# Kernel tuning notes

Measured on AMD Instinct MI355X. Metric: run time of the kernel, lower is better.

## Reference

```python
import jax, jax.numpy as jnp
import numpy as np

B, N, C, HEADS, SR = 4, 16384, 64, 2, 8
SIDE = 128            # sqrt(N)
NKV = (SIDE // SR) ** 2  # 256
D = C // HEADS
LN_EPS = 1e-5


def setup_inputs() -> dict:
    key = jax.random.key(0)
    ks = jax.random.split(key, 12)
    s = 0.02
    return {
        "x": jax.random.normal(ks[0], (B, N, C), jnp.float32),
        "pos_2D": jax.random.uniform(ks[1], (B, HEADS, N, NKV), jnp.float32),
        "q_w": jax.random.normal(ks[2], (C, C), jnp.float32) * s,
        "q_b": jnp.zeros((C,), jnp.float32),
        "kv_w": jax.random.normal(ks[3], (2 * C, C), jnp.float32) * s,
        "kv_b": jnp.zeros((2 * C,), jnp.float32),
        "proj_w": jax.random.normal(ks[4], (C, C), jnp.float32) * s,
        "proj_b": jnp.zeros((C,), jnp.float32),
        "sr_w": jax.random.normal(ks[5], (C, C, SR, SR), jnp.float32) * s,  # OIHW
        "sr_b": jnp.zeros((C,), jnp.float32),
        "ln_g": jnp.ones((C,), jnp.float32),
        "ln_b": jnp.zeros((C,), jnp.float32),
        "alpha": jnp.full((1,), 0.3, jnp.float32),
    }


def reference(x, pos_2D, q_w, q_b, kv_w, kv_b, proj_w, proj_b, sr_w, sr_b, ln_g, ln_b, alpha):
    scale = D ** -0.5
    # q projection -> [B, HEADS, N, D]
    q = (jnp.einsum("bnc,oc->bno", x, q_w) + q_b).reshape(B, N, HEADS, D).transpose(0, 2, 1, 3)
    # spatial reduction: conv stride SR on [B, C, SIDE, SIDE]
    xs = x.transpose(0, 2, 1).reshape(B, C, SIDE, SIDE)
    xs = jax.lax.conv_general_dilated(
        xs, sr_w, window_strides=(SR, SR), padding="VALID",
        dimension_numbers=("NCHW", "OIHW", "NCHW")) + sr_b[None, :, None, None]
    xs = xs.reshape(B, C, NKV).transpose(0, 2, 1)  # [B, NKV, C]
    # LayerNorm over channels
    mu = jnp.mean(xs, axis=-1, keepdims=True)
    var = jnp.mean(jnp.square(xs - mu), axis=-1, keepdims=True)
    xs = (xs - mu) * jax.lax.rsqrt(var + LN_EPS) * ln_g + ln_b
    # kv projection -> k, v each [B, HEADS, NKV, D]
    kv = (jnp.einsum("bmc,oc->bmo", xs, kv_w) + kv_b).reshape(B, NKV, 2, HEADS, D)
    kv = kv.transpose(2, 0, 3, 1, 4)
    k, v = kv[0], kv[1]
    # attention with post-softmax positional blend
    attn = jax.nn.softmax(jnp.einsum("bhnd,bhmd->bhnm", q, k) * scale, axis=-1)
    a = alpha[0]
    attn = (1.0 - a) * attn + a * pos_2D
    out = jnp.einsum("bhnm,bhmd->bhnd", attn, v)
    out = out.transpose(0, 2, 1, 3).reshape(B, N, C)
    return jnp.einsum("bnc,oc->bno", out, proj_w) + proj_b
```

## Files before the change

### kernel.cpp

```cpp
#include <hip/hip_runtime.h>
#include <cstdint>
#include <cstddef>

#define NN 16384
#define CC 64
#define LN_EPS 1e-5f

typedef __attribute__((ext_vector_type(8))) short short8;
typedef __attribute__((ext_vector_type(4))) float f32x4;
typedef unsigned short ushort_t;
typedef unsigned int uint32;

__device__ __forceinline__ ushort_t f2bf(float f) {
  union { float f; uint32 u; } v; v.f = f;
  return (ushort_t)((v.u + 0x8000u) >> 16);
}
__device__ __forceinline__ uint32 pk2(float a, float b) {
  union { float f; uint32 u; } x, y; x.f = a; y.f = b;
  return ((x.u + 0x8000u) >> 16) | ((y.u + 0x8000u) & 0xffff0000u);
}
__device__ __forceinline__ short8 pk8(float4 a, float4 b) {
  union { short8 s; uint32 u[4]; } r;
  r.u[0] = pk2(a.x, a.y); r.u[1] = pk2(a.z, a.w);
  r.u[2] = pk2(b.x, b.y); r.u[3] = pk2(b.z, b.w);
  return r.s;
}

__global__ void prep_kernel(const float* __restrict__ sr_w, float* __restrict__ w2T,
                            float* __restrict__ conv_acc) {
  int tid = blockIdx.x * 256 + threadIdx.x;
  if (tid < 64*64*64) {
    int j = tid >> 6, o = tid & 63;
    int i = j & 63, kw = (j >> 6) & 7, kh = j >> 9;
    w2T[tid] = sr_w[o*4096 + i*64 + kh*8 + kw];
  } else {
    int e = tid - 64*64*64;
    if (e < 1024*64) conv_acc[e] = 0.0f;
  }
}

__global__ __launch_bounds__(256) void conv_kernel(const float* __restrict__ x,
                                                   const float* __restrict__ w2T,
                                                   float* __restrict__ conv_acc) {
  __shared__ float A_lds[32*132];
  __shared__ float W_lds[128*64];
  int t = threadIdx.x;
  int pt = blockIdx.x >> 5, kc = blockIdx.x & 31;
  int kh = kc >> 2, kw0 = (kc & 3) * 2;
  const float4* wsrc = (const float4*)(w2T + kc*128*64);
  float4* wdst = (float4*)W_lds;
  #pragma unroll
  for (int v = 0; v < 8; ++v) wdst[t + v*256] = wsrc[t + v*256];
  #pragma unroll
  for (int v = 0; v < 4; ++v) {
    int idx = v*1024 + t*4;
    int pl = idx >> 7, off = idx & 127;
    int p = pt*32 + pl;
    int b = p >> 8, rem = p & 255, ph = rem >> 4, pw = rem & 15;
    int n0 = (ph*8 + kh)*128 + pw*8 + kw0;
    *(float4*)&A_lds[pl*132 + off] = *(const float4*)&x[(b*NN + n0)*CC + off];
  }
  __syncthreads();
  int og = t & 15, pp = t >> 4;
  float acc[8] = {0,0,0,0,0,0,0,0};
  #pragma unroll 8
  for (int k = 0; k < 128; ++k) {
    float4 w4 = *(const float4*)&W_lds[k*64 + og*4];
    float a0 = A_lds[pp*264 + k];
    float a1 = A_lds[pp*264 + 132 + k];
    acc[0] += a0*w4.x; acc[1] += a0*w4.y; acc[2] += a0*w4.z; acc[3] += a0*w4.w;
    acc[4] += a1*w4.x; acc[5] += a1*w4.y; acc[6] += a1*w4.z; acc[7] += a1*w4.w;
  }
  int p0 = pt*32 + pp*2;
  #pragma unroll
  for (int j2 = 0; j2 < 4; ++j2) {
    atomicAdd(&conv_acc[p0*64 + og*4 + j2], acc[j2]);
    atomicAdd(&conv_acc[(p0+1)*64 + og*4 + j2], acc[4+j2]);
  }
}

__global__ __launch_bounds__(256) void lnkv_kernel(const float* __restrict__ conv_acc,
    const float* __restrict__ sr_b, const float* __restrict__ ln_g, const float* __restrict__ ln_b,
    const float* __restrict__ kv_w, const float* __restrict__ kv_b,
    ushort_t* __restrict__ k_out, ushort_t* __restrict__ v_out) {
  __shared__ float xsrow[4][64];
  int t = threadIdx.x;
  int w = t >> 6, lane = t & 63;
  float4 wk[16], wv[16];
  #pragma unroll
  for (int c4 = 0; c4 < 16; ++c4) {
    wk[c4] = *(const float4*)&kv_w[lane*64 + c4*4];
    wv[c4] = *(const float4*)&kv_w[(64+lane)*64 + c4*4];
  }
  float kb0 = kv_b[lane], kb1 = kv_b[64+lane];
  float sb = sr_b[lane], lg = ln_g[lane], lb = ln_b[lane];
  int h = lane >> 5, dd = lane & 31;
  for (int i = 0; i < 8; ++i) {
    int row = blockIdx.x*32 + w*8 + i;
    float xc = conv_acc[row*64 + lane] + sb;
    float s = xc;
    #pragma unroll
    for (int m = 1; m < 64; m <<= 1) s += __shfl_xor(s, m);
    float mu = s * (1.0f/64.0f);
    float d0 = xc - mu;
    float vs = d0*d0;
    #pragma unroll
    for (int m = 1; m < 64; m <<= 1) vs += __shfl_xor(vs, m);
    float rs = rsqrtf(vs*(1.0f/64.0f) + LN_EPS);
    xsrow[w][lane] = d0*rs*lg + lb;
    __syncthreads();
    float acc0 = kb0, acc1 = kb1;
    #pragma unroll
    for (int c4 = 0; c4 < 16; ++c4) {
      float4 xv = *(const float4*)&xsrow[w][c4*4];
      acc0 += xv.x*wk[c4].x + xv.y*wk[c4].y + xv.z*wk[c4].z + xv.w*wk[c4].w;
      acc1 += xv.x*wv[c4].x + xv.y*wv[c4].y + xv.z*wv[c4].z + xv.w*wv[c4].w;
    }
    int b = row >> 8, m2 = row & 255;
    int bh = b*2 + h;
    k_out[(bh*256 + m2)*32 + dd] = f2bf(acc0);
    v_out[(bh*32 + dd)*256 + m2] = f2bf(acc1);
    __syncthreads();
  }
}

__global__ __launch_bounds__(256) void qproj_kernel(const float* __restrict__ x,
    const float* __restrict__ q_w, const float* __restrict__ q_b, ushort_t* __restrict__ q_out) {
  int t = threadIdx.x;
  int w = t >> 6, lane = t & 63;
  int quad = lane >> 4, col = lane & 15;
  const float qscale = 0.17677669529663687f * 1.4426950408889634f;
  short8 bf[4][2];
  float qb[4];
  #pragma unroll
  for (int ct = 0; ct < 4; ++ct) {
    #pragma unroll
    for (int ksb = 0; ksb < 2; ++ksb) {
      const float* src = &q_w[(ct*16 + col)*64 + ksb*32 + quad*8];
      bf[ct][ksb] = pk8(*(const float4*)src, *(const float4*)(src + 4));
    }
    qb[ct] = q_b[ct*16 + col];
  }
  int rows0 = blockIdx.x*64 + w*16;
  int arow = rows0 + col;
  const float* xs = &x[(size_t)arow*64];
  short8 af0 = pk8(*(const float4*)&xs[quad*8],      *(const float4*)&xs[quad*8 + 4]);
  short8 af1 = pk8(*(const float4*)&xs[32 + quad*8], *(const float4*)&xs[36 + quad*8]);
  const f32x4 zero = {0.f, 0.f, 0.f, 0.f};
  #pragma unroll
  for (int ct = 0; ct < 4; ++ct) {
    f32x4 acc = __builtin_amdgcn_mfma_f32_16x16x32_bf16(af0, bf[ct][0], zero, 0, 0, 0);
    acc = __builtin_amdgcn_mfma_f32_16x16x32_bf16(af1, bf[ct][1], acc, 0, 0, 0);
    int o = ct*16 + col;
    int bh_hi = o >> 5, dd = o & 31;
    #pragma unroll
    for (int r = 0; r < 4; ++r) {
      int gr = rows0 + quad*4 + r;
      int b = gr >> 14, n = gr & 16383;
      q_out[((size_t)(b*2 + bh_hi)*NN + n)*32 + dd] = f2bf((acc[r] + qb[ct]) * qscale);
    }
  }
}

__global__ __launch_bounds__(256, 2) void attn_kernel(const ushort_t* __restrict__ q_ws,
    const ushort_t* __restrict__ k_ws, const ushort_t* __restrict__ v_ws,
    const float* __restrict__ pos, const float* __restrict__ alpha,
    ushort_t* __restrict__ attnout) {
  __shared__ __align__(16) ushort_t k_lds[256*40];
  __shared__ __align__(16) ushort_t v_lds[32*264];
  __shared__ __align__(16) ushort_t p_lds[4][16*256];
  int t = threadIdx.x;
  int bh = blockIdx.x >> 6, blk = blockIdx.x & 63;
  int b = bh >> 1, h = bh & 1;
  {
    const uint4* ksrc = (const uint4*)(k_ws + bh*8192);
    const uint4* vsrc = (const uint4*)(v_ws + bh*8192);
    uint4* kd = (uint4*)k_lds; uint4* vd = (uint4*)v_lds;
    #pragma unroll
    for (int vv = 0; vv < 4; ++vv) {
      int i = t + vv*256;
      kd[(i >> 2)*5 + (i & 3)] = ksrc[i];
      vd[(i >> 5)*33 + (i & 31)] = vsrc[i];
    }
  }
  __syncthreads();
  int w = t >> 6, lane = t & 63, quad = lane >> 4, col = lane & 15;
  float a = alpha[0];
  float one_minus_a = 1.0f - a;
  const f32x4 zero = {0.f, 0.f, 0.f, 0.f};
  for (int it = 0; it < 4; ++it) {
    int n0 = blk*256 + (it*4 + w)*16;
    short8 qa = *(const short8*)&q_ws[((size_t)bh*NN + n0 + col)*32 + quad*8];
    f32x4 st[16];
    #pragma unroll
    for (int tt = 0; tt < 16; ++tt) {
      short8 kb = *(const short8*)&k_lds[(tt*16 + col)*40 + quad*8];
      st[tt] = __builtin_amdgcn_mfma_f32_16x16x32_bf16(qa, kb, zero, 0, 0, 0);
    }
    #pragma unroll
    for (int r = 0; r < 4; ++r) {
      float mx = st[0][r];
      #pragma unroll
      for (int tt = 1; tt < 16; ++tt) mx = fmaxf(mx, st[tt][r]);
      #pragma unroll
      for (int m = 1; m < 16; m <<= 1) mx = fmaxf(mx, __shfl_xor(mx, m));
      float sum = 0.f;
      #pragma unroll
      for (int tt = 0; tt < 16; ++tt) {
        float e = __builtin_amdgcn_exp2f(st[tt][r] - mx);
        st[tt][r] = e; sum += e;
      }
      #pragma unroll
      for (int m = 1; m < 16; m <<= 1) sum += __shfl_xor(sum, m);
      float coef = one_minus_a * __builtin_amdgcn_rcpf(sum);
      int row = quad*4 + r;
      #pragma unroll
      for (int tt = 0; tt < 16; ++tt) {
        float av = st[tt][r]*coef;
        int colg = tt*16 + col;
        int u = colg >> 3, within = colg & 7;
        int usw = u ^ (row & 7);
        p_lds[w][row*256 + usw*8 + within] = f2bf(av);
      }
    }
    float4 p4[16];
    const float* pbase = &pos[((size_t)bh*NN + n0 + col)*256 + quad*8];
    #pragma unroll
    for (int ks = 0; ks < 8; ++ks) {
      p4[ks*2]   = *(const float4*)(pbase + ks*32);
      p4[ks*2+1] = *(const float4*)(pbase + ks*32 + 4);
    }
    __syncthreads();
    f32x4 o0 = zero, o1 = zero, e0 = zero, e1 = zero;
    #pragma unroll
    for (int ks = 0; ks < 8; ++ks) {
      short8 pa  = *(const short8*)&p_lds[w][col*256 + (((ks*4 + quad) ^ (col & 7))*8)];
      short8 vb0 = *(const short8*)&v_lds[(col)*264 + ks*32 + quad*8];
      short8 vb1 = *(const short8*)&v_lds[(16 + col)*264 + ks*32 + quad*8];
      short8 pf  = pk8(p4[ks*2], p4[ks*2+1]);
      o0 = __builtin_amdgcn_mfma_f32_16x16x32_bf16(pa, vb0, o0, 0, 0, 0);
      o1 = __builtin_amdgcn_mfma_f32_16x16x32_bf16(pa, vb1, o1, 0, 0, 0);
      e0 = __builtin_amdgcn_mfma_f32_16x16x32_bf16(pf, vb0, e0, 0, 0, 0);
      e1 = __builtin_amdgcn_mfma_f32_16x16x32_bf16(pf, vb1, e1, 0, 0, 0);
    }
    #pragma unroll
    for (int r = 0; r < 4; ++r) {
      int q_row = n0 + quad*4 + r;
      int base = (b*NN + q_row)*64 + h*32;
      attnout[base + col]      = f2bf(o0[r] + a*e0[r]);
      attnout[base + 16 + col] = f2bf(o1[r] + a*e1[r]);
    }
  }
}

__global__ __launch_bounds__(256) void proj_kernel(const ushort_t* __restrict__ attnout,
    const float* __restrict__ proj_w, const float* __restrict__ proj_b, float* __restrict__ out) {
  int t = threadIdx.x;
  int w = t >> 6, lane = t & 63;
  int quad = lane >> 4, col = lane & 15;
  short8 bf[4][2];
  float pb[4];
  #pragma unroll
  for (int ct = 0; ct < 4; ++ct) {
    #pragma unroll
    for (int ksb = 0; ksb < 2; ++ksb) {
      const float* src = &proj_w[(ct*16 + col)*64 + ksb*32 + quad*8];
      bf[ct][ksb] = pk8(*(const float4*)src, *(const float4*)(src + 4));
    }
    pb[ct] = proj_b[ct*16 + col];
  }
  int rows0 = blockIdx.x*64 + w*16;
  int arow = rows0 + col;
  short8 af0 = *(const short8*)&attnout[(size_t)arow*64 + quad*8];
  short8 af1 = *(const short8*)&attnout[(size_t)arow*64 + 32 + quad*8];
  const f32x4 zero = {0.f, 0.f, 0.f, 0.f};
  #pragma unroll
  for (int ct = 0; ct < 4; ++ct) {
    f32x4 acc = __builtin_amdgcn_mfma_f32_16x16x32_bf16(af0, bf[ct][0], zero, 0, 0, 0);
    acc = __builtin_amdgcn_mfma_f32_16x16x32_bf16(af1, bf[ct][1], acc, 0, 0, 0);
    int o = ct*16 + col;
    #pragma unroll
    for (int r = 0; r < 4; ++r) {
      int gr = rows0 + quad*4 + r;
      out[(size_t)gr*64 + o] = acc[r] + pb[ct];
    }
  }
}

extern "C" void kernel_launch(void* const* d_in, const int* in_sizes, int n_in,
                              void* d_out, int out_size, void* d_ws, size_t ws_size,
                              hipStream_t stream) {
  const float* x      = (const float*)d_in[0];
  const float* pos    = (const float*)d_in[1];
  const float* q_w    = (const float*)d_in[2];
  const float* q_b    = (const float*)d_in[3];
  const float* kv_w   = (const float*)d_in[4];
  const float* kv_b   = (const float*)d_in[5];
  const float* proj_w = (const float*)d_in[6];
  const float* proj_b = (const float*)d_in[7];
  const float* sr_w   = (const float*)d_in[8];
  const float* sr_b   = (const float*)d_in[9];
  const float* ln_g   = (const float*)d_in[10];
  const float* ln_b   = (const float*)d_in[11];
  const float* alpha  = (const float*)d_in[12];
  float* out = (float*)d_out;

  char* ws = (char*)d_ws;
  float* conv_acc   = (float*)(ws);
  float* w2T        = (float*)(ws + (256u<<10));
  ushort_t* k_ws    = (ushort_t*)(ws + (1280u<<10));
  ushort_t* v_ws    = (ushort_t*)(ws + (1408u<<10));
  ushort_t* q_ws    = (ushort_t*)(ws + (1536u<<10));
  ushort_t* a_ws    = (ushort_t*)(ws + (9728u<<10));

  hipLaunchKernelGGL(prep_kernel,  dim3(1280), dim3(256), 0, stream, sr_w, w2T, conv_acc);
  hipLaunchKernelGGL(conv_kernel,  dim3(1024), dim3(256), 0, stream, x, w2T, conv_acc);
  hipLaunchKernelGGL(lnkv_kernel,  dim3(32),   dim3(256), 0, stream, conv_acc, sr_b, ln_g, ln_b, kv_w, kv_b, k_ws, v_ws);
  hipLaunchKernelGGL(qproj_kernel, dim3(1024), dim3(256), 0, stream, x, q_w, q_b, q_ws);
  hipLaunchKernelGGL(attn_kernel,  dim3(512),  dim3(256), 0, stream, q_ws, k_ws, v_ws, pos, alpha, a_ws);
  hipLaunchKernelGGL(proj_kernel,  dim3(1024), dim3(256), 0, stream, a_ws, proj_w, proj_b, out);
}
```

Before: 301.8 us.

## Replace conv atomics with partial buffers and coalesce q/attn/proj stores via LDS

The conv kernel now writes per-kernel-chunk partial sums to a 32-way partial buffer, and the LN/KV kernel reduces them, instead of using float atomics on a zeroed accumulator. q-projection, attention output and projection outputs are staged through LDS tiles so global stores become 16-byte coalesced writes. The attention output layout changes to per-head [bh,N,32], which proj reads. The pos_2D loads are hoisted ahead of the QK/softmax phase to overlap their latency, and a block barrier is removed. The trade-off is more workspace traffic (8MB of partials), a serial 32-way read in lnkv, and extra LDS usage in attention.

```diff
diff --git a/kernel.cpp b/kernel.cpp
--- a/kernel.cpp
+++ b/kernel.cpp
@@ -26,22 +26,16 @@
   return r.s;
 }
 
-__global__ void prep_kernel(const float* __restrict__ sr_w, float* __restrict__ w2T,
-                            float* __restrict__ conv_acc) {
+__global__ void prep_kernel(const float* __restrict__ sr_w, float* __restrict__ w2T) {
   int tid = blockIdx.x * 256 + threadIdx.x;
-  if (tid < 64*64*64) {
-    int j = tid >> 6, o = tid & 63;
-    int i = j & 63, kw = (j >> 6) & 7, kh = j >> 9;
-    w2T[tid] = sr_w[o*4096 + i*64 + kh*8 + kw];
-  } else {
-    int e = tid - 64*64*64;
-    if (e < 1024*64) conv_acc[e] = 0.0f;
-  }
+  int j = tid >> 6, o = tid & 63;
+  int i = j & 63, kw = (j >> 6) & 7, kh = j >> 9;
+  w2T[tid] = sr_w[o*4096 + i*64 + kh*8 + kw];
 }
 
 __global__ __launch_bounds__(256) void conv_kernel(const float* __restrict__ x,
                                                    const float* __restrict__ w2T,
-                                                   float* __restrict__ conv_acc) {
+                                                   float* __restrict__ part) {
   __shared__ float A_lds[32*132];
   __shared__ float W_lds[128*64];
   int t = threadIdx.x;
@@ -72,14 +66,14 @@
     acc[4] += a1*w4.x; acc[5] += a1*w4.y; acc[6] += a1*w4.z; acc[7] += a1*w4.w;
   }
   int p0 = pt*32 + pp*2;
-  #pragma unroll
-  for (int j2 = 0; j2 < 4; ++j2) {
-    atomicAdd(&conv_acc[p0*64 + og*4 + j2], acc[j2]);
-    atomicAdd(&conv_acc[(p0+1)*64 + og*4 + j2], acc[4+j2]);
-  }
-}
-
-__global__ __launch_bounds__(256) void lnkv_kernel(const float* __restrict__ conv_acc,
+  float* dst = &part[(size_t)kc*65536 + p0*64 + og*4];
+  float4 s0 = {acc[0], acc[1], acc[2], acc[3]};
+  float4 s1 = {acc[4], acc[5], acc[6], acc[7]};
+  *(float4*)dst = s0;
+  *(float4*)(dst + 64) = s1;
+}
+
+__global__ __launch_bounds__(256) void lnkv_kernel(const float* __restrict__ part,
     const float* __restrict__ sr_b, const float* __restrict__ ln_g, const float* __restrict__ ln_b,
     const float* __restrict__ kv_w, const float* __restrict__ kv_b,
     ushort_t* __restrict__ k_out, ushort_t* __restrict__ v_out) {
@@ -95,9 +89,11 @@
   float kb0 = kv_b[lane], kb1 = kv_b[64+lane];
   float sb = sr_b[lane], lg = ln_g[lane], lb = ln_b[lane];
   int h = lane >> 5, dd = lane & 31;
-  for (int i = 0; i < 8; ++i) {
-    int row = blockIdx.x*32 + w*8 + i;
-    float xc = conv_acc[row*64 + lane] + sb;
+  for (int i = 0; i < 2; ++i) {
+    int row = blockIdx.x*8 + w*2 + i;
+    float xc = sb;
+    #pragma unroll
+    for (int kc = 0; kc < 32; ++kc) xc += part[kc*65536 + row*64 + lane];
     float s = xc;
     #pragma unroll
     for (int m = 1; m < 64; m <<= 1) s += __shfl_xor(s, m);
@@ -108,7 +104,6 @@
     for (int m = 1; m < 64; m <<= 1) vs += __shfl_xor(vs, m);
     float rs = rsqrtf(vs*(1.0f/64.0f) + LN_EPS);
     xsrow[w][lane] = d0*rs*lg + lb;
-    __syncthreads();
     float acc0 = kb0, acc1 = kb1;
     #pragma unroll
     for (int c4 = 0; c4 < 16; ++c4) {
@@ -120,45 +115,51 @@
     int bh = b*2 + h;
     k_out[(bh*256 + m2)*32 + dd] = f2bf(acc0);
     v_out[(bh*32 + dd)*256 + m2] = f2bf(acc1);
-    __syncthreads();
   }
 }
 
 __global__ __launch_bounds__(256) void qproj_kernel(const float* __restrict__ x,
     const float* __restrict__ q_w, const float* __restrict__ q_b, ushort_t* __restrict__ q_out) {
+  __shared__ __align__(16) ushort_t q_tile[64*64];
   int t = threadIdx.x;
   int w = t >> 6, lane = t & 63;
   int quad = lane >> 4, col = lane & 15;
   const float qscale = 0.17677669529663687f * 1.4426950408889634f;
-  short8 bf[4][2];
+  short8 bfr[4][2];
   float qb[4];
   #pragma unroll
   for (int ct = 0; ct < 4; ++ct) {
     #pragma unroll
     for (int ksb = 0; ksb < 2; ++ksb) {
       const float* src = &q_w[(ct*16 + col)*64 + ksb*32 + quad*8];
-      bf[ct][ksb] = pk8(*(const float4*)src, *(const float4*)(src + 4));
+      bfr[ct][ksb] = pk8(*(const float4*)src, *(const float4*)(src + 4));
     }
     qb[ct] = q_b[ct*16 + col];
   }
-  int rows0 = blockIdx.x*64 + w*16;
-  int arow = rows0 + col;
+  int rows0 = blockIdx.x*64;
+  int arow = rows0 + w*16 + col;
   const float* xs = &x[(size_t)arow*64];
   short8 af0 = pk8(*(const float4*)&xs[quad*8],      *(const float4*)&xs[quad*8 + 4]);
   short8 af1 = pk8(*(const float4*)&xs[32 + quad*8], *(const float4*)&xs[36 + quad*8]);
   const f32x4 zero = {0.f, 0.f, 0.f, 0.f};
   #pragma unroll
   for (int ct = 0; ct < 4; ++ct) {
-    f32x4 acc = __builtin_amdgcn_mfma_f32_16x16x32_bf16(af0, bf[ct][0], zero, 0, 0, 0);
-    acc = __builtin_amdgcn_mfma_f32_16x16x32_bf16(af1, bf[ct][1], acc, 0, 0, 0);
-    int o = ct*16 + col;
-    int bh_hi = o >> 5, dd = o & 31;
-    #pragma unroll
-    for (int r = 0; r < 4; ++r) {
-      int gr = rows0 + quad*4 + r;
-      int b = gr >> 14, n = gr & 16383;
-      q_out[((size_t)(b*2 + bh_hi)*NN + n)*32 + dd] = f2bf((acc[r] + qb[ct]) * qscale);
-    }
+    f32x4 acc = __builtin_amdgcn_mfma_f32_16x16x32_bf16(af0, bfr[ct][0], zero, 0, 0, 0);
+    acc = __builtin_amdgcn_mfma_f32_16x16x32_bf16(af1, bfr[ct][1], acc, 0, 0, 0);
+    #pragma unroll
+    for (int r = 0; r < 4; ++r)
+      q_tile[(w*16 + quad*4 + r)*64 + ct*16 + col] = f2bf((acc[r] + qb[ct]) * qscale);
+  }
+  __syncthreads();
+  int u = t;
+  #pragma unroll
+  for (int s = 0; s < 2; ++s, u += 256) {
+    int row = u >> 3, seg = u & 7;
+    int h2 = seg >> 2, sg = seg & 3;
+    uint4 val = *(const uint4*)&q_tile[row*64 + seg*8];
+    int gr = rows0 + row;
+    int b2 = gr >> 14, n = gr & 16383;
+    *(uint4*)&q_out[((size_t)(b2*2 + h2)*NN + n)*32 + sg*8] = val;
   }
 }
 
@@ -169,9 +170,9 @@
   __shared__ __align__(16) ushort_t k_lds[256*40];
   __shared__ __align__(16) ushort_t v_lds[32*264];
   __shared__ __align__(16) ushort_t p_lds[4][16*256];
+  __shared__ __align__(16) ushort_t o_lds[4][16*32];
   int t = threadIdx.x;
   int bh = blockIdx.x >> 6, blk = blockIdx.x & 63;
-  int b = bh >> 1, h = bh & 1;
   {
     const uint4* ksrc = (const uint4*)(k_ws + bh*8192);
     const uint4* vsrc = (const uint4*)(v_ws + bh*8192);
@@ -190,6 +191,13 @@
   const f32x4 zero = {0.f, 0.f, 0.f, 0.f};
   for (int it = 0; it < 4; ++it) {
     int n0 = blk*256 + (it*4 + w)*16;
+    float4 p4[16];
+    const float* pbase = &pos[((size_t)bh*NN + n0 + col)*256 + quad*8];
+    #pragma unroll
+    for (int ks = 0; ks < 8; ++ks) {
+      p4[ks*2]   = *(const float4*)(pbase + ks*32);
+      p4[ks*2+1] = *(const float4*)(pbase + ks*32 + 4);
+    }
     short8 qa = *(const short8*)&q_ws[((size_t)bh*NN + n0 + col)*32 + quad*8];
     f32x4 st[16];
     #pragma unroll
@@ -223,14 +231,6 @@
         p_lds[w][row*256 + usw*8 + within] = f2bf(av);
       }
     }
-    float4 p4[16];
-    const float* pbase = &pos[((size_t)bh*NN + n0 + col)*256 + quad*8];
-    #pragma unroll
-    for (int ks = 0; ks < 8; ++ks) {
-      p4[ks*2]   = *(const float4*)(pbase + ks*32);
-      p4[ks*2+1] = *(const float4*)(pbase + ks*32 + 4);
-    }
-    __syncthreads();
     f32x4 o0 = zero, o1 = zero, e0 = zero, e1 = zero;
     #pragma unroll
     for (int ks = 0; ks < 8; ++ks) {
@@ -245,45 +245,54 @@
     }
     #pragma unroll
     for (int r = 0; r < 4; ++r) {
-      int q_row = n0 + quad*4 + r;
-      int base = (b*NN + q_row)*64 + h*32;
-      attnout[base + col]      = f2bf(o0[r] + a*e0[r]);
-      attnout[base + 16 + col] = f2bf(o1[r] + a*e1[r]);
-    }
+      int row = quad*4 + r;
+      o_lds[w][row*32 + col]      = f2bf(o0[r] + a*e0[r]);
+      o_lds[w][row*32 + 16 + col] = f2bf(o1[r] + a*e1[r]);
+    }
+    int rowu = lane >> 2, seg = lane & 3;
+    uint4 val = *(const uint4*)&o_lds[w][rowu*32 + seg*8];
+    *(uint4*)&attnout[((size_t)bh*NN + n0 + rowu)*32 + seg*8] = val;
   }
 }
 
 __global__ __launch_bounds__(256) void proj_kernel(const ushort_t* __restrict__ attnout,
     const float* __restrict__ proj_w, const float* __restrict__ proj_b, float* __restrict__ out) {
+  __shared__ __align__(16) float o_tile[64*68];
   int t = threadIdx.x;
   int w = t >> 6, lane = t & 63;
   int quad = lane >> 4, col = lane & 15;
-  short8 bf[4][2];
+  short8 bfr[4][2];
   float pb[4];
   #pragma unroll
   for (int ct = 0; ct < 4; ++ct) {
     #pragma unroll
     for (int ksb = 0; ksb < 2; ++ksb) {
       const float* src = &proj_w[(ct*16 + col)*64 + ksb*32 + quad*8];
-      bf[ct][ksb] = pk8(*(const float4*)src, *(const float4*)(src + 4));
+      bfr[ct][ksb] = pk8(*(const float4*)src, *(const float4*)(src + 4));
     }
     pb[ct] = proj_b[ct*16 + col];
   }
-  int rows0 = blockIdx.x*64 + w*16;
-  int arow = rows0 + col;
-  short8 af0 = *(const short8*)&attnout[(size_t)arow*64 + quad*8];
-  short8 af1 = *(const short8*)&attnout[(size_t)arow*64 + 32 + quad*8];
+  int rows0 = blockIdx.x*64;
+  int arow = rows0 + w*16 + col;
+  int b2 = arow >> 14, n = arow & 16383;
+  short8 af0 = *(const short8*)&attnout[((size_t)(b2*2)*NN + n)*32 + quad*8];
+  short8 af1 = *(const short8*)&attnout[((size_t)(b2*2 + 1)*NN + n)*32 + quad*8];
   const f32x4 zero = {0.f, 0.f, 0.f, 0.f};
   #pragma unroll
   for (int ct = 0; ct < 4; ++ct) {
-    f32x4 acc = __builtin_amdgcn_mfma_f32_16x16x32_bf16(af0, bf[ct][0], zero, 0, 0, 0);
-    acc = __builtin_amdgcn_mfma_f32_16x16x32_bf16(af1, bf[ct][1], acc, 0, 0, 0);
-    int o = ct*16 + col;
-    #pragma unroll
-    for (int r = 0; r < 4; ++r) {
-      int gr = rows0 + quad*4 + r;
-      out[(size_t)gr*64 + o] = acc[r] + pb[ct];
-    }
+    f32x4 acc = __builtin_amdgcn_mfma_f32_16x16x32_bf16(af0, bfr[ct][0], zero, 0, 0, 0);
+    acc = __builtin_amdgcn_mfma_f32_16x16x32_bf16(af1, bfr[ct][1], acc, 0, 0, 0);
+    #pragma unroll
+    for (int r = 0; r < 4; ++r)
+      o_tile[(w*16 + quad*4 + r)*68 + ct*16 + col] = acc[r] + pb[ct];
+  }
+  __syncthreads();
+  int u = t;
+  #pragma unroll
+  for (int s = 0; s < 4; ++s, u += 256) {
+    int row = u >> 4, c4 = u & 15;
+    float4 val = *(const float4*)&o_tile[row*68 + c4*4];
+    *(float4*)&out[(size_t)(rows0 + row)*64 + c4*4] = val;
   }
 }
 
@@ -306,16 +315,16 @@
   float* out = (float*)d_out;
 
   char* ws = (char*)d_ws;
-  float* conv_acc   = (float*)(ws);
-  float* w2T        = (float*)(ws + (256u<<10));
-  ushort_t* k_ws    = (ushort_t*)(ws + (1280u<<10));
-  ushort_t* v_ws    = (ushort_t*)(ws + (1408u<<10));
-  ushort_t* q_ws    = (ushort_t*)(ws + (1536u<<10));
-  ushort_t* a_ws    = (ushort_t*)(ws + (9728u<<10));
-
-  hipLaunchKernelGGL(prep_kernel,  dim3(1280), dim3(256), 0, stream, sr_w, w2T, conv_acc);
-  hipLaunchKernelGGL(conv_kernel,  dim3(1024), dim3(256), 0, stream, x, w2T, conv_acc);
-  hipLaunchKernelGGL(lnkv_kernel,  dim3(32),   dim3(256), 0, stream, conv_acc, sr_b, ln_g, ln_b, kv_w, kv_b, k_ws, v_ws);
+  float* part       = (float*)(ws);
+  float* w2T        = (float*)(ws + (8u<<20));
+  ushort_t* k_ws    = (ushort_t*)(ws + (9u<<20));
+  ushort_t* v_ws    = (ushort_t*)(ws + (9u<<20) + (128u<<10));
+  ushort_t* q_ws    = (ushort_t*)(ws + (10u<<20));
+  ushort_t* a_ws    = (ushort_t*)(ws + (18u<<20));
+
+  hipLaunchKernelGGL(prep_kernel,  dim3(1024), dim3(256), 0, stream, sr_w, w2T);
+  hipLaunchKernelGGL(conv_kernel,  dim3(1024), dim3(256), 0, stream, x, w2T, part);
+  hipLaunchKernelGGL(lnkv_kernel,  dim3(128),  dim3(256), 0, stream, part, sr_b, ln_g, ln_b, kv_w, kv_b, k_ws, v_ws);
   hipLaunchKernelGGL(qproj_kernel, dim3(1024), dim3(256), 0, stream, x, q_w, q_b, q_ws);
   hipLaunchKernelGGL(attn_kernel,  dim3(512),  dim3(256), 0, stream, q_ws, k_ws, v_ws, pos, alpha, a_ws);
   hipLaunchKernelGGL(proj_kernel,  dim3(1024), dim3(256), 0, stream, a_ws, proj_w, proj_b, out);
```

Measured after the change: 277.3 us. 1.09x faster.
